# Performance work log

Hardware: AMD Instinct MI355X
Metric: run time of the kernel (lower is better)

Reference implementation:

```python
import jax, jax.numpy as jnp
import numpy as np

REWARD_SCALE = 1.0
DIST_NORM = 2
LATENT_DIST_THRESHOLD = 6.0

BS, N_VIEWS, N_PART, F_DIM = 128, 4, 1024, 10


def setup_inputs() -> dict:
    key = jax.random.key(0)
    k1, k2, k3, k4 = jax.random.split(key, 4)
    achieved_goal = jax.random.normal(k1, (BS, N_VIEWS, N_PART, F_DIM), jnp.float32)
    desired_goal = jax.random.normal(k2, (BS, N_VIEWS, N_PART, F_DIM), jnp.float32)
    norm_mean = jax.random.normal(k3, (F_DIM,), jnp.float32)
    norm_std = jax.random.uniform(k4, (F_DIM,), jnp.float32, minval=0.5, maxval=1.5)
    return {"achieved_goal": achieved_goal, "desired_goal": desired_goal,
            "norm_mean": norm_mean, "norm_std": norm_std}


def _pairwise_sqdist(x, y):
    # x: [bs, n, d], y: [bs, m, d] -> [bs, n, m] squared L2 ('l2_simple')
    xx = jnp.sum(x * x, axis=-1)            # [bs, n]
    yy = jnp.sum(y * y, axis=-1)            # [bs, m]
    xy = jnp.einsum('bnd,bmd->bnm', x, y)   # [bs, n, m]
    return xx[:, :, None] + yy[:, None, :] - 2.0 * xy


def _particle_mask(particles):
    # latent_classifier is None -> obj_class_cond = ones -> mask = (1 == 0) = all False
    obj_on = particles[..., -1]
    return jnp.zeros_like(obj_on, dtype=bool)


def reference(achieved_goal, desired_goal, norm_mean, norm_std):
    # unnormalize (particle_normalizer.unnormalize modeled as affine)
    state_particles = achieved_goal * norm_std + norm_mean
    goal_particles = desired_goal * norm_std + norm_mean
    bs, n_views, n_particles, _ = state_particles.shape

    state_mask = _particle_mask(state_particles)   # [bs, nv, np] bool
    goal_mask = _particle_mask(goal_particles)

    # P_mask[b,v,i,j] = state_mask[b,v,i] | goal_mask[b,v,j]
    P_mask = jnp.logical_or(state_mask[..., :, None], goal_mask[..., None, :])

    state_vis = state_particles[..., 5:9]
    state_xy = state_particles[..., :2]
    goal_vis = goal_particles[..., 5:9]
    goal_xy = goal_particles[..., :2]

    inf = jnp.asarray(jnp.inf, state_particles.dtype)
    rewards = []
    for i in range(n_views):
        sxy = state_xy[:, i]                 # [bs, np, 2]
        gxy = goal_xy[:, i]
        gmask_i = goal_mask[:, i]            # [bs, np]
        smask_i = state_mask[:, i]

        P = _pairwise_sqdist(state_vis[:, i], goal_vis[:, i])  # [bs, np_state, np_goal]
        P = jnp.where(P_mask[:, i], inf, P)

        # goal -> state direction: min over state dim (axis 1)
        min_d1 = jnp.min(P, axis=1)                            # [bs, np_goal]
        idx1 = jnp.argmin(P, axis=1)                           # [bs, np_goal]
        d_goal = jnp.take_along_axis(sxy, idx1[..., None], axis=1)  # [bs, np_goal, 2]
        xy_dist_1 = jnp.linalg.norm(gxy - d_goal, ord=DIST_NORM, axis=-1)
        xy_dist_1 = jnp.where(min_d1 > LATENT_DIST_THRESHOLD, 1.0, xy_dist_1)
        xy_dist_1 = jnp.where(gmask_i, 0.0, xy_dist_1)
        n_obj_g = jnp.maximum(jnp.sum(~gmask_i, axis=1), 1)
        reward_g2s = -jnp.sum(xy_dist_1, axis=1) / n_obj_g

        # state -> goal direction: min over goal dim (axis 2)
        min_d2 = jnp.min(P, axis=2)
        idx2 = jnp.argmin(P, axis=2)
        d_state = jnp.take_along_axis(gxy, idx2[..., None], axis=1)
        xy_dist_2 = jnp.linalg.norm(sxy - d_state, ord=DIST_NORM, axis=-1)
        xy_dist_2 = jnp.where(min_d2 > LATENT_DIST_THRESHOLD, 1.0, xy_dist_2)
        xy_dist_2 = jnp.where(smask_i, 0.0, xy_dist_2)
        n_obj_s = jnp.maximum(jnp.sum(~smask_i, axis=1), 1)
        reward_s2g = -jnp.sum(xy_dist_2, axis=1) / n_obj_s

        rv = (reward_g2s + reward_s2g) / 2.0
        no_valid = jnp.logical_or(jnp.all(gmask_i, axis=-1), jnp.all(smask_i, axis=-1))
        rv = jnp.where(no_valid, -1.0, rv)
        rewards.append(rv)

    reward = jnp.mean(jnp.stack(rewards, axis=0), axis=0)   # [bs]
    return REWARD_SCALE * reward[:, None]                    # [bs, 1]
```

## Files before the change

### kernel.cpp

```cpp
#include <hip/hip_runtime.h>
#include <cstdint>
#include <cstddef>

#define NP    1024
#define FD    10
#define NV    4
#define BSZ   128
#define NPAIR (BSZ * NV)
#define NSET  (NPAIR * 2)
#define TPB   256
#define RPT   2

#define OFF_CS   16777216
#define OFF_PART 20971520


extern "C" __global__ __launch_bounds__(256)
void chamfer_stage(const float* __restrict__ ag, const float* __restrict__ dg,
                   const float* __restrict__ nmean, const float* __restrict__ nstd,
                   float* __restrict__ vis2o, float* __restrict__ cso)
{
    const int s   = blockIdx.x;
    const int tid = threadIdx.x;
    const float* src = ((s & 1) ? ag : dg) + (size_t)(s >> 1) * (NP * FD);
    float st[4], mn[4];
#pragma unroll
    for (int j = 0; j < 4; ++j) {
        st[j] = -2.0f * nstd[5 + j];
        mn[j] = -2.0f * nmean[5 + j];
    }
    float4* vout = (float4*)vis2o + (size_t)s * NP;
    float*  cout = cso + (size_t)s * NP;
    for (int n = tid; n < NP; n += 256) {
        const float* p = src + (size_t)n * FD + 5;
        float v0 = fmaf(p[0], st[0], mn[0]);
        float v1 = fmaf(p[1], st[1], mn[1]);
        float v2 = fmaf(p[2], st[2], mn[2]);
        float v3 = fmaf(p[3], st[3], mn[3]);
        vout[n] = make_float4(v0, v1, v2, v3);
        cout[n] = 0.25f * (v0 * v0 + v1 * v1 + v2 * v2 + v3 * v3);
    }
}

extern "C" __global__ __launch_bounds__(TPB, 8)
void chamfer_pairs(const float* __restrict__ vis2, const float* __restrict__ cs,
                   const float* __restrict__ ag, const float* __restrict__ dg,
                   const float* __restrict__ nmean, const float* __restrict__ nstd,
                   float* __restrict__ partial )
{
    __shared__ float redbuf[TPB / 64];

    const int bid  = blockIdx.x;
    const int pd   = bid >> 1;
    const int half = bid & 1;
    const int pair = pd >> 1;
    const int d    = pd & 1;
    const int tid  = threadIdx.x;

    const float4* cvis  = (const float4*)vis2 + (size_t)pd * NP;
    const float*  ccs   = cs + (size_t)pd * NP;
    const float4* rvis4 = (const float4*)vis2 + (size_t)(pd ^ 1) * NP;
    const float*  rcs   = cs + (size_t)(pd ^ 1) * NP;

    const float* rxyg = ((d == 0) ? ag : dg) + (size_t)pair * (NP * FD);
    const float* cxyg = ((d == 0) ? dg : ag) + (size_t)pair * (NP * FD);

    float4 rv[RPT];
    float  rthr[RPT];
    float  bestd[RPT];
    int    bblk[RPT];
#pragma unroll
    for (int r = 0; r < RPT; ++r) {
        int n = half * 512 + tid + TPB * r;
        float4 t = rvis4[n];
        rv[r] = make_float4(-0.5f * t.x, -0.5f * t.y, -0.5f * t.z, -0.5f * t.w);
        rthr[r] = 6.0f - rcs[n];
        bestd[r] = 3.0e38f;
        bblk[r]  = 0;
    }

    for (int m = 0; m < NP; m += 8) {
        float4 c0 = cvis[m + 0];
        float4 c1 = cvis[m + 1];
        float4 c2 = cvis[m + 2];
        float4 c3 = cvis[m + 3];
        float4 c4 = cvis[m + 4];
        float4 c5 = cvis[m + 5];
        float4 c6 = cvis[m + 6];
        float4 c7 = cvis[m + 7];
        float4 csA = *(const float4*)(ccs + m);
        float4 csB = *(const float4*)(ccs + m + 4);
#pragma unroll
        for (int r = 0; r < RPT; ++r) {
            float4 v = rv[r];
            float d0 = fmaf(v.x, c0.x, csA.x); d0 = fmaf(v.y, c0.y, d0); d0 = fmaf(v.z, c0.z, d0); d0 = fmaf(v.w, c0.w, d0);
            float d1 = fmaf(v.x, c1.x, csA.y); d1 = fmaf(v.y, c1.y, d1); d1 = fmaf(v.z, c1.z, d1); d1 = fmaf(v.w, c1.w, d1);
            float d2 = fmaf(v.x, c2.x, csA.z); d2 = fmaf(v.y, c2.y, d2); d2 = fmaf(v.z, c2.z, d2); d2 = fmaf(v.w, c2.w, d2);
            float d3 = fmaf(v.x, c3.x, csA.w); d3 = fmaf(v.y, c3.y, d3); d3 = fmaf(v.z, c3.z, d3); d3 = fmaf(v.w, c3.w, d3);
            float d4 = fmaf(v.x, c4.x, csB.x); d4 = fmaf(v.y, c4.y, d4); d4 = fmaf(v.z, c4.z, d4); d4 = fmaf(v.w, c4.w, d4);
            float d5 = fmaf(v.x, c5.x, csB.y); d5 = fmaf(v.y, c5.y, d5); d5 = fmaf(v.z, c5.z, d5); d5 = fmaf(v.w, c5.w, d5);
            float d6 = fmaf(v.x, c6.x, csB.z); d6 = fmaf(v.y, c6.y, d6); d6 = fmaf(v.z, c6.z, d6); d6 = fmaf(v.w, c6.w, d6);
            float d7 = fmaf(v.x, c7.x, csB.w); d7 = fmaf(v.y, c7.y, d7); d7 = fmaf(v.z, c7.z, d7); d7 = fmaf(v.w, c7.w, d7);
            float p0 = fminf(fminf(d0, d1), d2);
            float p1 = fminf(fminf(d3, d4), d5);
            float p2 = fminf(d6, d7);
            float bm = fminf(fminf(p0, p1), p2);
            bool lt = bm < bestd[r];
            bestd[r] = fminf(bestd[r], bm);
            bblk[r]  = lt ? m : bblk[r];
        }
    }

    const float std0 = nstd[0], mean0 = nmean[0];
    const float std1 = nstd[1], mean1 = nmean[1];
    float sum = 0.0f;
#pragma unroll
    for (int r = 0; r < RPT; ++r) {
        int n  = half * 512 + tid + TPB * r;
        int mb = bblk[r];
        float4 v = rv[r];
        float4 csA = *(const float4*)(ccs + mb);
        float4 csB = *(const float4*)(ccs + mb + 4);
        float cse[8] = {csA.x, csA.y, csA.z, csA.w, csB.x, csB.y, csB.z, csB.w};
        float dd[8];
#pragma unroll
        for (int j = 0; j < 8; ++j) {
            float4 c = cvis[mb + j];
            float t = fmaf(v.x, c.x, cse[j]);
            t = fmaf(v.y, c.y, t);
            t = fmaf(v.z, c.z, t);
            t = fmaf(v.w, c.w, t);
            dd[j] = t;
        }
        int sel = 0;
#pragma unroll
        for (int j = 7; j >= 0; --j)
            if (dd[j] == bestd[r]) sel = j;
        int idx = mb + sel;

        float gx = fmaf(cxyg[(size_t)idx * FD + 0], std0, mean0);
        float gy = fmaf(cxyg[(size_t)idx * FD + 1], std1, mean1);
        float ax = fmaf(rxyg[(size_t)n * FD + 0], std0, mean0);
        float ay = fmaf(rxyg[(size_t)n * FD + 1], std1, mean1);
        float dx = ax - gx;
        float dy = ay - gy;
        float dist = sqrtf(dx * dx + dy * dy);
        if (bestd[r] > rthr[r]) dist = 1.0f;
        sum += dist;
    }

    for (int o = 32; o > 0; o >>= 1) sum += __shfl_down(sum, o, 64);
    if ((tid & 63) == 0) redbuf[tid >> 6] = sum;
    __syncthreads();
    if (tid == 0) {
        float s = redbuf[0] + redbuf[1] + redbuf[2] + redbuf[3];
        partial[bid] = s;
    }
}

extern "C" __global__ void chamfer_final(const float* __restrict__ partial,
                                         float* __restrict__ out)
{
    int b = threadIdx.x;
    if (b < BSZ) {
        float s = 0.0f;
#pragma unroll
        for (int i = 0; i < 16; ++i) s += partial[b * 16 + i];
        out[b] = s * (-1.0f / 8192.0f);
    }
}

extern "C" void kernel_launch(void* const* d_in, const int* in_sizes, int n_in,
                              void* d_out, int out_size, void* d_ws, size_t ws_size,
                              hipStream_t stream)
{
    const float* ag = (const float*)d_in[0];
    const float* dg = (const float*)d_in[1];
    const float* nm = (const float*)d_in[2];
    const float* ns = (const float*)d_in[3];

    char*  ws      = (char*)d_ws;
    float* vis2    = (float*)(ws);
    float* csbuf   = (float*)(ws + OFF_CS);
    float* partial = (float*)(ws + OFF_PART);

    chamfer_stage<<<NSET, 256, 0, stream>>>(ag, dg, nm, ns, vis2, csbuf);
    chamfer_pairs<<<NSET * 2, TPB, 0, stream>>>(vis2, csbuf, ag, dg, nm, ns, partial);
    chamfer_final<<<1, BSZ, 0, stream>>>(partial, (float*)d_out);
}
```

Measured before the change: 256.3 us.

## Stage particles via LDS, use constant-address loads, fuse final reduction with atomics

The staging kernel now copies each particle set into shared memory with coalesced float4 loads and then extracts the visual features, replacing strided global reads. The pairwise kernel reads the column features through address-space-4 (constant) pointers so the compiler can emit scalar loads for the wave-uniform data. The final reduction kernel is removed: blocks atomically add their scaled partial sums into the zeroed output. This saves a launch but makes the floating-point summation order nondeterministic.

After: 256.7 us. Within noise of the previous version (+0.1%).

```diff
diff --git a/kernel.cpp b/kernel.cpp
--- a/kernel.cpp
+++ b/kernel.cpp
@@ -6,13 +6,14 @@
 #define FD    10
 #define NV    4
 #define BSZ   128
-#define NPAIR (BSZ * NV)
-#define NSET  (NPAIR * 2)
+#define NSET  1024
 #define TPB   256
 #define RPT   2
 
-#define OFF_CS   16777216
-#define OFF_PART 20971520
+#define OFF_CS 16777216
+
+typedef float fv4 __attribute__((ext_vector_type(4)));
+typedef const fv4 __attribute__((address_space(4)))* c4p;
 
 
 extern "C" __global__ __launch_bounds__(256)
@@ -20,24 +21,30 @@
                    const float* __restrict__ nmean, const float* __restrict__ nstd,
                    float* __restrict__ vis2o, float* __restrict__ cso)
 {
+    __shared__ float raw[NP * FD];
     const int s   = blockIdx.x;
     const int tid = threadIdx.x;
-    const float* src = ((s & 1) ? ag : dg) + (size_t)(s >> 1) * (NP * FD);
-    float st[4], mn[4];
+    const float4* src = (const float4*)(((s & 1) ? ag : dg) + (size_t)(s >> 1) * (NP * FD));
+    float4* lraw = (float4*)raw;
 #pragma unroll
-    for (int j = 0; j < 4; ++j) {
-        st[j] = -2.0f * nstd[5 + j];
-        mn[j] = -2.0f * nmean[5 + j];
-    }
-    float4* vout = (float4*)vis2o + (size_t)s * NP;
-    float*  cout = cso + (size_t)s * NP;
+    for (int i = 0; i < 10; ++i)
+        lraw[tid + 256 * i] = src[tid + 256 * i];
+
+    float st0 = -2.0f * nstd[5], mn0 = -2.0f * nmean[5];
+    float st1 = -2.0f * nstd[6], mn1 = -2.0f * nmean[6];
+    float st2 = -2.0f * nstd[7], mn2 = -2.0f * nmean[7];
+    float st3 = -2.0f * nstd[8], mn3 = -2.0f * nmean[8];
+    __syncthreads();
+
+    fv4*   vout = (fv4*)vis2o + (size_t)s * NP;
+    float* cout = cso + (size_t)s * NP;
     for (int n = tid; n < NP; n += 256) {
-        const float* p = src + (size_t)n * FD + 5;
-        float v0 = fmaf(p[0], st[0], mn[0]);
-        float v1 = fmaf(p[1], st[1], mn[1]);
-        float v2 = fmaf(p[2], st[2], mn[2]);
-        float v3 = fmaf(p[3], st[3], mn[3]);
-        vout[n] = make_float4(v0, v1, v2, v3);
+        float v0 = fmaf(raw[FD * n + 5], st0, mn0);
+        float v1 = fmaf(raw[FD * n + 6], st1, mn1);
+        float v2 = fmaf(raw[FD * n + 7], st2, mn2);
+        float v3 = fmaf(raw[FD * n + 8], st3, mn3);
+        fv4 v; v.x = v0; v.y = v1; v.z = v2; v.w = v3;
+        vout[n] = v;
         cout[n] = 0.25f * (v0 * v0 + v1 * v1 + v2 * v2 + v3 * v3);
     }
 }
@@ -46,7 +53,7 @@
 void chamfer_pairs(const float* __restrict__ vis2, const float* __restrict__ cs,
                    const float* __restrict__ ag, const float* __restrict__ dg,
                    const float* __restrict__ nmean, const float* __restrict__ nstd,
-                   float* __restrict__ partial )
+                   float* __restrict__ out )
 {
     __shared__ float redbuf[TPB / 64];
 
@@ -57,9 +64,11 @@
     const int d    = pd & 1;
     const int tid  = threadIdx.x;
 
-    const float4* cvis  = (const float4*)vis2 + (size_t)pd * NP;
-    const float*  ccs   = cs + (size_t)pd * NP;
-    const float4* rvis4 = (const float4*)vis2 + (size_t)(pd ^ 1) * NP;
+    c4p cvisS = (c4p)(uintptr_t)(vis2 + (size_t)pd * NP * 4);
+    c4p ccsS  = (c4p)(uintptr_t)(cs   + (size_t)pd * NP);
+    const float4* cvisV = (const float4*)(vis2 + (size_t)pd * NP * 4);
+    const float*  ccsV  = cs + (size_t)pd * NP;
+    const float4* rvis4 = (const float4*)(vis2 + (size_t)(pd ^ 1) * NP * 4);
     const float*  rcs   = cs + (size_t)(pd ^ 1) * NP;
 
     const float* rxyg = ((d == 0) ? ag : dg) + (size_t)pair * (NP * FD);
@@ -79,17 +88,18 @@
         bblk[r]  = 0;
     }
 
-    for (int m = 0; m < NP; m += 8) {
-        float4 c0 = cvis[m + 0];
-        float4 c1 = cvis[m + 1];
-        float4 c2 = cvis[m + 2];
-        float4 c3 = cvis[m + 3];
-        float4 c4 = cvis[m + 4];
-        float4 c5 = cvis[m + 5];
-        float4 c6 = cvis[m + 6];
-        float4 c7 = cvis[m + 7];
-        float4 csA = *(const float4*)(ccs + m);
-        float4 csB = *(const float4*)(ccs + m + 4);
+    for (int mb8 = 0; mb8 < NP / 8; ++mb8) {
+        const int m = mb8 * 8;
+        fv4 c0 = cvisS[m + 0];
+        fv4 c1 = cvisS[m + 1];
+        fv4 c2 = cvisS[m + 2];
+        fv4 c3 = cvisS[m + 3];
+        fv4 c4 = cvisS[m + 4];
+        fv4 c5 = cvisS[m + 5];
+        fv4 c6 = cvisS[m + 6];
+        fv4 c7 = cvisS[m + 7];
+        fv4 csA = ccsS[mb8 * 2 + 0];
+        fv4 csB = ccsS[mb8 * 2 + 1];
 #pragma unroll
         for (int r = 0; r < RPT; ++r) {
             float4 v = rv[r];
@@ -119,13 +129,13 @@
         int n  = half * 512 + tid + TPB * r;
         int mb = bblk[r];
         float4 v = rv[r];
-        float4 csA = *(const float4*)(ccs + mb);
-        float4 csB = *(const float4*)(ccs + mb + 4);
-        float cse[8] = {csA.x, csA.y, csA.z, csA.w, csB.x, csB.y, csB.z, csB.w};
+        float cse[8];
+#pragma unroll
+        for (int j = 0; j < 8; ++j) cse[j] = ccsV[mb + j];
         float dd[8];
 #pragma unroll
         for (int j = 0; j < 8; ++j) {
-            float4 c = cvis[mb + j];
+            float4 c = cvisV[mb + j];
             float t = fmaf(v.x, c.x, cse[j]);
             t = fmaf(v.y, c.y, t);
             t = fmaf(v.z, c.z, t);
@@ -154,19 +164,7 @@
     __syncthreads();
     if (tid == 0) {
         float s = redbuf[0] + redbuf[1] + redbuf[2] + redbuf[3];
-        partial[bid] = s;
-    }
-}
-
-extern "C" __global__ void chamfer_final(const float* __restrict__ partial,
-                                         float* __restrict__ out)
-{
-    int b = threadIdx.x;
-    if (b < BSZ) {
-        float s = 0.0f;
-#pragma unroll
-        for (int i = 0; i < 16; ++i) s += partial[b * 16 + i];
-        out[b] = s * (-1.0f / 8192.0f);
+        atomicAdd(&out[pair >> 2], s * (-1.0f / 8192.0f));
     }
 }
 
@@ -179,12 +177,11 @@
     const float* nm = (const float*)d_in[2];
     const float* ns = (const float*)d_in[3];
 
-    char*  ws      = (char*)d_ws;
-    float* vis2    = (float*)(ws);
-    float* csbuf   = (float*)(ws + OFF_CS);
-    float* partial = (float*)(ws + OFF_PART);
+    char*  ws    = (char*)d_ws;
+    float* vis2  = (float*)(ws);
+    float* csbuf = (float*)(ws + OFF_CS);
 
+    hipMemsetAsync(d_out, 0, BSZ * sizeof(float), stream);
     chamfer_stage<<<NSET, 256, 0, stream>>>(ag, dg, nm, ns, vis2, csbuf);
-    chamfer_pairs<<<NSET * 2, TPB, 0, stream>>>(vis2, csbuf, ag, dg, nm, ns, partial);
-    chamfer_final<<<1, BSZ, 0, stream>>>(partial, (float*)d_out);
+    chamfer_pairs<<<NSET * 2, TPB, 0, stream>>>(vis2, csbuf, ag, dg, nm, ns, (float*)d_out);
 }
```
